# Optimization experiments

Measured on AMD Instinct MI355X. Metric: run time of the kernel, lower is better.

Reference implementation:

```python
import jax, jax.numpy as jnp
import numpy as np

B, H, S, D = 4, 16, 2048, 64


def setup_inputs() -> dict:
    key = jax.random.key(0)
    kq, kk, kv = jax.random.split(key, 3)
    q = jax.random.normal(kq, (B, H, S, D), dtype=jnp.float32)
    k = jax.random.normal(kk, (B, H, S, D), dtype=jnp.float32)
    v = jax.random.normal(kv, (B, H, S, D), dtype=jnp.float32)
    # causal mask, broadcastable over batch/heads (True = keep)
    mask = jnp.tril(jnp.ones((S, S), dtype=bool))[None, None, :, :]
    return {"q": q, "k": k, "v": v, "mask": mask}


def reference(q, k, v, mask):
    d_k = q.shape[-1]
    # [..., q, k] scores with full materialization, as in the original
    scores = jnp.einsum("bhqd,bhkd->bhqk", q, k) / jnp.sqrt(jnp.float32(d_k))
    scores = jnp.where(mask, scores, jnp.float32(-jnp.inf))
    attn = jax.nn.softmax(scores, axis=-1)  # stable: single max-subtract, matches manual softmax
    out = jnp.einsum("bhqk,bhkd->bhqd", attn, v)
    return out
```

## Files before the change

### kernel.cpp

```cpp
#include <hip/hip_runtime.h>
#include <hip/hip_bf16.h>
#include <stdint.h>

#define S_LEN 2048
#define D_DIM 64
#define BH    64
#define NQT   16
#define LOG2E 1.44269504088896f
#define THR   8.0f
#define TEN_ELEMS (BH * S_LEN * D_DIM)

typedef __attribute__((ext_vector_type(8)))  short bf16x8;
typedef __attribute__((ext_vector_type(4)))  short s16x4;
typedef __attribute__((ext_vector_type(4)))  float f32x4;
typedef __attribute__((ext_vector_type(16))) float f32x16;
typedef __attribute__((ext_vector_type(4)))  uint32_t u32x4;

__device__ __forceinline__ short f2bf(float f) {
    uint32_t u = __builtin_bit_cast(uint32_t, f);
    u += 0x7FFFu + ((u >> 16) & 1u);
    return (short)(u >> 16);
}

__device__ __forceinline__ uint32_t pkbf(float lo, float hi) {
    __hip_bfloat162 h = __float22bfloat162_rn(make_float2(lo, hi));
    uint32_t r;
    __builtin_memcpy(&r, &h, 4);
    return r;
}

__device__ __forceinline__ float xhalf_max(float v) {
    return fmaxf(v, __shfl_xor(v, 32));
}
__device__ __forceinline__ float xhalf_sum(float v) {
    return v + __shfl_xor(v, 32);
}

__device__ __forceinline__ int swz(int row, int col) {
    return (row * 64 + col) ^ ((row & 7) << 3);
}

#if __has_builtin(__builtin_amdgcn_exp2f)
#define EXP2(x) __builtin_amdgcn_exp2f(x)
#else
#define EXP2(x) exp2f(x)
#endif

__global__ __launch_bounds__(256)
void cvt_qk_kernel(const float* __restrict__ Q, const float* __restrict__ K,
                   short* __restrict__ Qb, short* __restrict__ Kb)
{
    const size_t off = ((size_t)blockIdx.x * 256 + threadIdx.x) * 8;
    const float sc = 0.125f * LOG2E;
    f32x4 a0 = *(const f32x4*)(Q + off), a1 = *(const f32x4*)(Q + off + 4);
    f32x4 b0 = *(const f32x4*)(K + off), b1 = *(const f32x4*)(K + off + 4);
    bf16x8 qa, kb;
    #pragma unroll
    for (int j = 0; j < 4; ++j) {
        qa[j] = f2bf(a0[j] * sc); qa[4 + j] = f2bf(a1[j] * sc);
        kb[j] = f2bf(b0[j]);      kb[4 + j] = f2bf(b1[j]);
    }
    *(bf16x8*)(Qb + off) = qa;
    *(bf16x8*)(Kb + off) = kb;
}

__global__ __launch_bounds__(256)
void vt_kernel(const float* __restrict__ V, short* __restrict__ Vt)
{
    const int kt = blockIdx.x;
    const int bh = blockIdx.y;
    const float* Vp = V + (size_t)bh * S_LEN * D_DIM + (size_t)kt * 64 * D_DIM;
    short* Vo = Vt + (size_t)bh * D_DIM * S_LEN;
    __shared__ short T[64][72];
    const int tid = threadIdx.x;
    const int row = tid >> 2, q4 = tid & 3;
    #pragma unroll
    for (int j = 0; j < 4; ++j) {
        f32x4 v = *(const f32x4*)(Vp + row * D_DIM + q4 * 16 + j * 4);
        #pragma unroll
        for (int e = 0; e < 4; ++e) T[row][q4 * 16 + j * 4 + e] = f2bf(v[e]);
    }
    __syncthreads();
    const int d = tid >> 2, kq = tid & 3;
    #pragma unroll
    for (int j = 0; j < 4; ++j) {
        s16x4 w;
        #pragma unroll
        for (int e = 0; e < 4; ++e) w[e] = T[kq * 16 + j * 4 + e][d];
        *(s16x4*)&Vo[(size_t)d * S_LEN + kt * 64 + kq * 16 + j * 4] = w;
    }
}

#define ISSUE_B(kb) do { \
    const short* kp_ = Kp + (size_t)(kb) * 64 * D_DIM; \
    const short* vp_ = Vtp + (kb) * 64; \
    _Pragma("unroll") for (int it = 0; it < 4; ++it) { \
        const int idx_ = tid + it * 256; \
        const int row_ = idx_ >> 4, c4_ = idx_ & 15; \
        kreg[it] = *(const s16x4*)(kp_ + row_ * D_DIM + c4_ * 4); \
        vreg[it] = *(const s16x4*)(vp_ + (size_t)row_ * S_LEN + c4_ * 4); \
    } \
} while (0)

#define WRITE_LDS_B(b) do { \
    _Pragma("unroll") for (int it = 0; it < 4; ++it) { \
        const int idx_ = tid + it * 256; \
        const int row_ = idx_ >> 4, c4_ = idx_ & 15; \
        *(s16x4*)&Kl[b][swz(row_, c4_ * 4)] = kreg[it]; \
        *(s16x4*)&Vl[b][swz(row_, c4_ * 4)] = vreg[it]; \
    } \
} while (0)

#define MKFRAG(dst, sv, R0) do { \
    uint32_t x_ = pkbf(sv[(R0)+0], sv[(R0)+1]), y_ = pkbf(sv[(R0)+2], sv[(R0)+3]); \
    uint32_t u_ = pkbf(sv[(R0)+4], sv[(R0)+5]), v_ = pkbf(sv[(R0)+6], sv[(R0)+7]); \
    const uint32_t px_ = (uint32_t)__shfl_xor((int)x_, 32); \
    const uint32_t py_ = (uint32_t)__shfl_xor((int)y_, 32); \
    const uint32_t pu_ = (uint32_t)__shfl_xor((int)u_, 32); \
    const uint32_t pv_ = (uint32_t)__shfl_xor((int)v_, 32); \
    u32x4 t_; \
    t_[0] = hi ? pu_ : x_;  t_[1] = hi ? pv_ : y_; \
    t_[2] = hi ? u_  : px_; t_[3] = hi ? v_  : py_; \
    dst = __builtin_bit_cast(bf16x8, t_); \
} while (0)

#define PVSTEP(pa, koff, acc0, acc1, b) do { \
    bf16x8 vf0_ = *(const bf16x8*)&Vl[b][swz(lq32,      (koff) + hi * 8)]; \
    bf16x8 vf1_ = *(const bf16x8*)&Vl[b][swz(32 + lq32, (koff) + hi * 8)]; \
    acc0 = __builtin_amdgcn_mfma_f32_32x32x16_bf16(pa, vf0_, acc0, 0, 0, 0); \
    acc1 = __builtin_amdgcn_mfma_f32_32x32x16_bf16(pa, vf1_, acc1, 0, 0, 0); \
} while (0)

#define COMPUTE32(qf, acc0, acc1, mm, ll, q0, kv0, b) do { \
    f32x16 s0_ = (f32x16)0.f, s1_ = (f32x16)0.f; \
    _Pragma("unroll") for (int c = 0; c < 4; ++c) { \
        bf16x8 k0_ = *(const bf16x8*)&Kl[b][swz(lq32,      c * 16 + hi * 8)]; \
        bf16x8 k1_ = *(const bf16x8*)&Kl[b][swz(32 + lq32, c * 16 + hi * 8)]; \
        s0_ = __builtin_amdgcn_mfma_f32_32x32x16_bf16(k0_, qf[c], s0_, 0, 0, 0); \
        s1_ = __builtin_amdgcn_mfma_f32_32x32x16_bf16(k1_, qf[c], s1_, 0, 0, 0); \
    } \
    if ((kv0) + 63 > (q0)) {    \
        _Pragma("unroll") for (int r = 0; r < 16; ++r) { \
            const int kvr_ = (r & 3) + 8 * (r >> 2) + 4 * hi; \
            if ((kv0) + kvr_      > (q0) + lq32) s0_[r] = -1e30f; \
            if ((kv0) + 32 + kvr_ > (q0) + lq32) s1_[r] = -1e30f; \
        } \
    } \
    float m0_ = fmaxf(s0_[0], s1_[0]), m1_ = fmaxf(s0_[1], s1_[1]); \
    float m2_ = fmaxf(s0_[2], s1_[2]), m3_ = fmaxf(s0_[3], s1_[3]); \
    _Pragma("unroll") for (int r = 4; r < 16; r += 4) { \
        m0_ = fmaxf(m0_, fmaxf(s0_[r],     s1_[r])); \
        m1_ = fmaxf(m1_, fmaxf(s0_[r + 1], s1_[r + 1])); \
        m2_ = fmaxf(m2_, fmaxf(s0_[r + 2], s1_[r + 2])); \
        m3_ = fmaxf(m3_, fmaxf(s0_[r + 3], s1_[r + 3])); \
    } \
    float pmax_ = xhalf_max(fmaxf(fmaxf(m0_, m1_), fmaxf(m2_, m3_))); \
    if (!__all(pmax_ <= (mm) + THR)) {       \
        const float mn_ = fmaxf((mm), pmax_); \
        const float f_  = EXP2((mm) - mn_); \
        (ll) *= f_; \
        _Pragma("unroll") for (int r = 0; r < 16; ++r) { \
            const float fr_ = __shfl(f_, (r & 3) + 8 * (r >> 2) + 4 * hi); \
            acc0[r] *= fr_; acc1[r] *= fr_; \
        } \
        (mm) = mn_; \
    } \
    float t0_ = 0.f, t1_ = 0.f, t2_ = 0.f, t3_ = 0.f; \
    _Pragma("unroll") for (int r = 0; r < 16; r += 4) { \
        s0_[r]     = EXP2(s0_[r]     - (mm)); s1_[r]     = EXP2(s1_[r]     - (mm)); \
        s0_[r + 1] = EXP2(s0_[r + 1] - (mm)); s1_[r + 1] = EXP2(s1_[r + 1] - (mm)); \
        s0_[r + 2] = EXP2(s0_[r + 2] - (mm)); s1_[r + 2] = EXP2(s1_[r + 2] - (mm)); \
        s0_[r + 3] = EXP2(s0_[r + 3] - (mm)); s1_[r + 3] = EXP2(s1_[r + 3] - (mm)); \
        t0_ += s0_[r]     + s1_[r]; \
        t1_ += s0_[r + 1] + s1_[r + 1]; \
        t2_ += s0_[r + 2] + s1_[r + 2]; \
        t3_ += s0_[r + 3] + s1_[r + 3]; \
    } \
    (ll) += (t0_ + t1_) + (t2_ + t3_);       \
    bf16x8 pa0_, pa1_, pa2_, pa3_; \
    MKFRAG(pa0_, s0_, 0); MKFRAG(pa1_, s0_, 8); \
    MKFRAG(pa2_, s1_, 0); MKFRAG(pa3_, s1_, 8); \
    PVSTEP(pa0_, 0,  acc0, acc1, b); \
    PVSTEP(pa1_, 16, acc0, acc1, b); \
    PVSTEP(pa2_, 32, acc0, acc1, b); \
    PVSTEP(pa3_, 48, acc0, acc1, b); \
} while (0)

__global__ __launch_bounds__(256, 2)
void attn_fwd_bf16(const short* __restrict__ Qb, const short* __restrict__ Kb,
                   const short* __restrict__ Vt, float* __restrict__ Out)
{
    const int bh   = blockIdx.x;
    const int pair = blockIdx.y;
    const int tid  = threadIdx.x;
    const int wid  = tid >> 6;
    const int lane = tid & 63;
    const int lq32 = lane & 31;
    const int hi   = lane >> 5;

    const int qtA = NQT - 1 - pair;
    const int qtB = pair;
    const int nkv = 2 * qtA + 2;

    const short* Qp  = Qb + (size_t)bh * S_LEN * D_DIM;
    const short* Kp  = Kb + (size_t)bh * S_LEN * D_DIM;
    const short* Vtp = Vt + (size_t)bh * D_DIM * S_LEN;
    float*       Op  = Out + (size_t)bh * S_LEN * D_DIM;

    __shared__ __align__(16) short Kl[2][64 * 64];
    __shared__ __align__(16) short Vl[2][64 * 64];

    const int q0A = qtA * 128 + wid * 32;
    const int q0B = qtB * 128 + wid * 32;

    bf16x8 qfA[4], qfB[4];
    #pragma unroll
    for (int c = 0; c < 4; ++c) {
        qfA[c] = *(const bf16x8*)(Qp + (size_t)(q0A + lq32) * D_DIM + c * 16 + hi * 8);
        qfB[c] = *(const bf16x8*)(Qp + (size_t)(q0B + lq32) * D_DIM + c * 16 + hi * 8);
    }

    f32x16 accA0 = (f32x16)0.f, accA1 = (f32x16)0.f;
    f32x16 accB0 = (f32x16)0.f, accB1 = (f32x16)0.f;
    float mA = -1e30f, lA = 0.f, mB = -1e30f, lB = 0.f;

    s16x4 kreg[4], vreg[4];

    ISSUE_B(0);
    WRITE_LDS_B(0);
    __syncthreads();

    for (int j = 0; j < nkv; ++j) {
        const int  kv0  = j * 64;
        const int  buf  = j & 1;
        const bool more = (j + 1) < nkv;
        if (more) ISSUE_B(j + 1);
        if (kv0 <= q0A + 31) COMPUTE32(qfA, accA0, accA1, mA, lA, q0A, kv0, buf);
        if (kv0 <= q0B + 31) COMPUTE32(qfB, accB0, accB1, mB, lB, q0B, kv0, buf);
        if (more) {
            WRITE_LDS_B(buf ^ 1);
            __syncthreads();
        }
    }

    lA = xhalf_sum(lA);
    lB = xhalf_sum(lB);
    const float iA = 1.f / lA;
    const float iB = 1.f / lB;
    #pragma unroll
    for (int r = 0; r < 16; ++r) {
        const int qr   = (r & 3) + 8 * (r >> 2) + 4 * hi;
        const float vA = __shfl(iA, qr);
        const float vB = __shfl(iB, qr);
        Op[(size_t)(q0A + qr) * D_DIM + lq32]      = accA0[r] * vA;
        Op[(size_t)(q0A + qr) * D_DIM + 32 + lq32] = accA1[r] * vA;
        Op[(size_t)(q0B + qr) * D_DIM + lq32]      = accB0[r] * vB;
        Op[(size_t)(q0B + qr) * D_DIM + 32 + lq32] = accB1[r] * vB;
    }
}

extern "C" void kernel_launch(void* const* d_in, const int* in_sizes, int n_in,
                              void* d_out, int out_size, void* d_ws, size_t ws_size,
                              hipStream_t stream) {
    const float* q = (const float*)d_in[0];
    const float* k = (const float*)d_in[1];
    const float* v = (const float*)d_in[2];
    float* out = (float*)d_out;
    (void)in_sizes; (void)n_in; (void)out_size; (void)ws_size;

    short* Qb = (short*)d_ws;
    short* Kb = Qb + TEN_ELEMS;
    short* Vt = Kb + TEN_ELEMS;
    cvt_qk_kernel<<<TEN_ELEMS / 8 / 256, 256, 0, stream>>>(q, k, Qb, Kb);
    vt_kernel<<<dim3(S_LEN / 64, BH), 256, 0, stream>>>(v, Vt);
    attn_fwd_bf16<<<dim3(BH, NQT / 2), 256, 0, stream>>>(Qb, Kb, Vt, out);
}
```

Measured before the change: 97.12 us.

## Replace paired causal q-tiles with one q-tile per block and MFMA priority hints

```diff
diff --git a/kernel.cpp b/kernel.cpp
--- a/kernel.cpp
+++ b/kernel.cpp
@@ -133,12 +133,14 @@
 
 #define COMPUTE32(qf, acc0, acc1, mm, ll, q0, kv0, b) do { \
     f32x16 s0_ = (f32x16)0.f, s1_ = (f32x16)0.f; \
+    __builtin_amdgcn_s_setprio(1); \
     _Pragma("unroll") for (int c = 0; c < 4; ++c) { \
         bf16x8 k0_ = *(const bf16x8*)&Kl[b][swz(lq32,      c * 16 + hi * 8)]; \
         bf16x8 k1_ = *(const bf16x8*)&Kl[b][swz(32 + lq32, c * 16 + hi * 8)]; \
         s0_ = __builtin_amdgcn_mfma_f32_32x32x16_bf16(k0_, qf[c], s0_, 0, 0, 0); \
         s1_ = __builtin_amdgcn_mfma_f32_32x32x16_bf16(k1_, qf[c], s1_, 0, 0, 0); \
     } \
+    __builtin_amdgcn_s_setprio(0); \
     if ((kv0) + 63 > (q0)) {    \
         _Pragma("unroll") for (int r = 0; r < 16; ++r) { \
             const int kvr_ = (r & 3) + 8 * (r >> 2) + 4 * hi; \
@@ -180,10 +182,12 @@
     bf16x8 pa0_, pa1_, pa2_, pa3_; \
     MKFRAG(pa0_, s0_, 0); MKFRAG(pa1_, s0_, 8); \
     MKFRAG(pa2_, s1_, 0); MKFRAG(pa3_, s1_, 8); \
+    __builtin_amdgcn_s_setprio(1); \
     PVSTEP(pa0_, 0,  acc0, acc1, b); \
     PVSTEP(pa1_, 16, acc0, acc1, b); \
     PVSTEP(pa2_, 32, acc0, acc1, b); \
     PVSTEP(pa3_, 48, acc0, acc1, b); \
+    __builtin_amdgcn_s_setprio(0); \
 } while (0)
 
 __global__ __launch_bounds__(256, 2)
@@ -191,16 +195,14 @@
                    const short* __restrict__ Vt, float* __restrict__ Out)
 {
     const int bh   = blockIdx.x;
-    const int pair = blockIdx.y;
+    const int qt   = NQT - 1 - blockIdx.y;
     const int tid  = threadIdx.x;
     const int wid  = tid >> 6;
     const int lane = tid & 63;
     const int lq32 = lane & 31;
     const int hi   = lane >> 5;
 
-    const int qtA = NQT - 1 - pair;
-    const int qtB = pair;
-    const int nkv = 2 * qtA + 2;
+    const int nkv = 2 * qt + 2;
 
     const short* Qp  = Qb + (size_t)bh * S_LEN * D_DIM;
     const short* Kp  = Kb + (size_t)bh * S_LEN * D_DIM;
@@ -210,19 +212,15 @@
     __shared__ __align__(16) short Kl[2][64 * 64];
     __shared__ __align__(16) short Vl[2][64 * 64];
 
-    const int q0A = qtA * 128 + wid * 32;
-    const int q0B = qtB * 128 + wid * 32;
-
-    bf16x8 qfA[4], qfB[4];
-    #pragma unroll
-    for (int c = 0; c < 4; ++c) {
-        qfA[c] = *(const bf16x8*)(Qp + (size_t)(q0A + lq32) * D_DIM + c * 16 + hi * 8);
-        qfB[c] = *(const bf16x8*)(Qp + (size_t)(q0B + lq32) * D_DIM + c * 16 + hi * 8);
-    }
-
-    f32x16 accA0 = (f32x16)0.f, accA1 = (f32x16)0.f;
-    f32x16 accB0 = (f32x16)0.f, accB1 = (f32x16)0.f;
-    float mA = -1e30f, lA = 0.f, mB = -1e30f, lB = 0.f;
+    const int q0 = qt * 128 + wid * 32;
+
+    bf16x8 qf[4];
+    #pragma unroll
+    for (int c = 0; c < 4; ++c)
+        qf[c] = *(const bf16x8*)(Qp + (size_t)(q0 + lq32) * D_DIM + c * 16 + hi * 8);
+
+    f32x16 acc0 = (f32x16)0.f, acc1 = (f32x16)0.f;
+    float m = -1e30f, l = 0.f;
 
     s16x4 kreg[4], vreg[4];
 
@@ -235,27 +233,21 @@
         const int  buf  = j & 1;
         const bool more = (j + 1) < nkv;
         if (more) ISSUE_B(j + 1);
-        if (kv0 <= q0A + 31) COMPUTE32(qfA, accA0, accA1, mA, lA, q0A, kv0, buf);
-        if (kv0 <= q0B + 31) COMPUTE32(qfB, accB0, accB1, mB, lB, q0B, kv0, buf);
+        if (kv0 <= q0 + 31) COMPUTE32(qf, acc0, acc1, m, l, q0, kv0, buf);
         if (more) {
             WRITE_LDS_B(buf ^ 1);
             __syncthreads();
         }
     }
 
-    lA = xhalf_sum(lA);
-    lB = xhalf_sum(lB);
-    const float iA = 1.f / lA;
-    const float iB = 1.f / lB;
+    l = xhalf_sum(l);
+    const float il = 1.f / l;
     #pragma unroll
     for (int r = 0; r < 16; ++r) {
         const int qr   = (r & 3) + 8 * (r >> 2) + 4 * hi;
-        const float vA = __shfl(iA, qr);
-        const float vB = __shfl(iB, qr);
-        Op[(size_t)(q0A + qr) * D_DIM + lq32]      = accA0[r] * vA;
-        Op[(size_t)(q0A + qr) * D_DIM + 32 + lq32] = accA1[r] * vA;
-        Op[(size_t)(q0B + qr) * D_DIM + lq32]      = accB0[r] * vB;
-        Op[(size_t)(q0B + qr) * D_DIM + 32 + lq32] = accB1[r] * vB;
+        const float vl = __shfl(il, qr);
+        Op[(size_t)(q0 + qr) * D_DIM + lq32]      = acc0[r] * vl;
+        Op[(size_t)(q0 + qr) * D_DIM + 32 + lq32] = acc1[r] * vl;
     }
 }
 
@@ -273,5 +265,5 @@
     short* Vt = Kb + TEN_ELEMS;
     cvt_qk_kernel<<<TEN_ELEMS / 8 / 256, 256, 0, stream>>>(q, k, Qb, Kb);
     vt_kernel<<<dim3(S_LEN / 64, BH), 256, 0, stream>>>(v, Vt);
-    attn_fwd_bf16<<<dim3(BH, NQT / 2), 256, 0, stream>>>(Qb, Kb, Vt, out);
-}
+    attn_fwd_bf16<<<dim3(BH, NQT), 256, 0, stream>>>(Qb, Kb, Vt, out);
+}
```

Result: faster. 91.08 us (-6.2%).
